# Kernel tuning notes

Measured on AMD Instinct MI355X. Metric: run time of the kernel, lower is better.

The kernel has to match this reference:

```python
import jax, jax.numpy as jnp
import numpy as np

N_NODES = 100000


def gcn_conv(x, W, b, src, dst, n_nodes):
    # PyG GCNConv: x' = D^{-1/2} (A + I) D^{-1/2} (x W) + b, deg counts self-loops
    h = x @ W  # [N, out]
    deg = jax.ops.segment_sum(jnp.ones_like(dst, dtype=h.dtype), dst, num_segments=n_nodes) + 1.0
    dinv = jax.lax.rsqrt(deg)  # [N]
    norm = dinv[src] * dinv[dst]  # per-edge norm [E]
    msg = h[src] * norm[:, None]  # gather + scale, [E, out]
    agg = jax.ops.segment_sum(msg, dst, num_segments=n_nodes)
    agg = agg + h * (dinv * dinv)[:, None]  # self-loop contribution
    return agg + b


def setup_inputs() -> dict:
    key = jax.random.key(0)
    ks = jax.random.split(key, 9)
    N, E, D = N_NODES, 3200000, 165
    x = jax.random.normal(ks[0], (N, D), dtype=jnp.float32)
    edge_index = jax.random.randint(ks[1], (2, E), 0, N, dtype=jnp.int64)
    def glorot(k, fan_in, fan_out):
        lim = np.sqrt(6.0 / (fan_in + fan_out))
        return jax.random.uniform(k, (fan_in, fan_out), jnp.float32, -lim, lim)
    return {
        "x": x,
        "edge_index": edge_index,
        "W1": glorot(ks[2], D, 32), "b1": jnp.zeros((32,), jnp.float32),
        "W2": glorot(ks[3], 32, 16), "b2": jnp.zeros((16,), jnp.float32),
        "W3": glorot(ks[4], 16, 2),  "b3": jnp.zeros((2,), jnp.float32),
    }


def reference(x, edge_index, W1, b1, W2, b2, W3, b3):
    src, dst = edge_index[0], edge_index[1]
    n = x.shape[0]
    h = jax.nn.relu(gcn_conv(x, W1, b1, src, dst, n))
    # dropout p=0.3 is a no-op in eval mode (training=False)
    h = jax.nn.relu(gcn_conv(h, W2, b2, src, dst, n))
    h = gcn_conv(h, W3, b3, src, dst, n)
    return jax.nn.log_softmax(h, axis=1)
```

## Files before the change

### kernel.cpp

```cpp
#include <hip/hip_runtime.h>
#include <math.h>


constexpr int NT = 256;
constexpr int NPB = 256;
constexpr int LOG_NPB = 8;
constexpr int MAXBUK = 512;
constexpr int BSTRIDE = 10240;
constexpr int NREP = 8;
constexpr int SUB = BSTRIDE / NREP;
constexpr int EPB_B = 4096;

typedef __attribute__((ext_vector_type(8))) short bf16x8;
typedef __attribute__((ext_vector_type(4))) float f32x4;

__device__ inline unsigned short f2bf(float f) {
    unsigned u = *(unsigned*)&f;
    u += 0x7fffu + ((u >> 16) & 1u);
    return (unsigned short)(u >> 16);
}
__device__ inline unsigned packbf(float a, float b) {
    return (unsigned)f2bf(a) | ((unsigned)f2bf(b) << 16);
}

__global__ __launch_bounds__(NT) void place_kernel(const int* __restrict__ src,
                                                   const int* __restrict__ dst,
                                                   int* __restrict__ cursor8,
                                                   unsigned* __restrict__ ebuf,
                                                   int E, int nbuk) {
    __shared__ int lh[MAXBUK];
    __shared__ int lbase[MAXBUK];
    for (int i = threadIdx.x; i < nbuk; i += NT) lh[i] = 0;
    __syncthreads();
    constexpr int EPT = EPB_B / NT;
    unsigned pk[EPT];
    unsigned bl[EPT];
    int base = blockIdx.x * EPB_B;
    int rep = blockIdx.x & (NREP - 1);
#pragma unroll
    for (int i = 0; i < EPT; i++) {
        int e = base + i * NT + threadIdx.x;
        if (e < E) {
            int s = src[e], d = dst[e];
            int b = d >> LOG_NPB;
            int lp = atomicAdd(&lh[b], 1);
            pk[i] = ((unsigned)(d & (NPB - 1)) << 24) | (unsigned)s;
            bl[i] = ((unsigned)b << 16) | (unsigned)lp;
        } else {
            bl[i] = 0xFFFFFFFFu;
        }
    }
    __syncthreads();
    for (int i = threadIdx.x; i < nbuk; i += NT) {
        int v = lh[i];
        if (v) lbase[i] = atomicAdd(&cursor8[rep * MAXBUK + i], v);
    }
    __syncthreads();
#pragma unroll
    for (int i = 0; i < EPT; i++) {
        if (bl[i] != 0xFFFFFFFFu) {
            int b = (int)(bl[i] >> 16);
            int pos = lbase[b] + (int)(bl[i] & 0xFFFFu);
            if (pos < SUB)
                ebuf[(size_t)b * BSTRIDE + rep * SUB + pos] = pk[i];
        }
    }
}

__global__ __launch_bounds__(NT) void sort_kernel(
    const unsigned* __restrict__ ebuf, const int* __restrict__ cursor8,
    int* __restrict__ esrc, int* __restrict__ rowptr, int* __restrict__ rowcnt,
    float* __restrict__ dinv, int N) {
    __shared__ int cnt[NPB];
    __shared__ int ofs[NPB];
    __shared__ int cur[NPB];
    int tid = threadIdx.x;
    int b = blockIdx.x;
    cnt[tid] = 0;
    __syncthreads();
#pragma unroll
    for (int r = 0; r < NREP; r++) {
        int e0 = b * BSTRIDE + r * SUB;
        int e1 = e0 + min(cursor8[r * MAXBUK + b], SUB);
        for (int i = e0 + tid; i < e1; i += NT)
            atomicAdd(&cnt[ebuf[i] >> 24], 1);
    }
    __syncthreads();
    ofs[tid] = cnt[tid];
    __syncthreads();
    for (int off = 1; off < NPB; off <<= 1) {
        int a = (tid >= off) ? ofs[tid - off] : 0;
        __syncthreads();
        ofs[tid] += a;
        __syncthreads();
    }
    {
        int excl = ofs[tid] - cnt[tid];
        cur[tid] = excl;
        int n = b * NPB + tid;
        if (n < N) {
            rowptr[n] = b * BSTRIDE + excl;
            rowcnt[n] = cnt[tid];
            dinv[n] = rsqrtf((float)cnt[tid] + 1.0f);
        }
    }
    __syncthreads();
#pragma unroll
    for (int r = 0; r < NREP; r++) {
        int e0 = b * BSTRIDE + r * SUB;
        int e1 = e0 + min(cursor8[r * MAXBUK + b], SUB);
        for (int i = e0 + tid; i < e1; i += NT) {
            unsigned p = ebuf[i];
            int l = (int)(p >> 24);
            int pos = atomicAdd(&cur[l], 1);
            esrc[b * BSTRIDE + pos] = (int)(p & 0xFFFFFFu);
        }
    }
}

__global__ __launch_bounds__(NT) void gemm1_mfma(
    const float* __restrict__ in, const float* __restrict__ W,
    const float* __restrict__ dinv, uint4* __restrict__ hs, int Ntot) {
    constexpr int DIN = 165, DOUT = 32;
    __shared__ float tile[4][16][36];
    int lane = threadIdx.x & 63;
    int wv = threadIdx.x >> 6;
    int t = blockIdx.x * 4 + wv;
    int ntiles = (Ntot + 15) >> 4;
    if (t >= ntiles) return;
    int n0 = t << 4;
    int mrow = lane & 15;
    int quad = lane >> 4;
    int arow = n0 + mrow;
    if (arow >= Ntot) arow = Ntot - 1;
    const float* xrow = in + (size_t)arow * DIN;
    f32x4 acc0 = {0.f, 0.f, 0.f, 0.f};
    f32x4 acc1 = {0.f, 0.f, 0.f, 0.f};
#pragma unroll
    for (int c = 0; c < 6; c++) {
        int kb = c * 32 + quad * 8;
        union { bf16x8 v; unsigned short u[8]; } A, B0, B1;
#pragma unroll
        for (int j = 0; j < 8; j++) {
            int k = kb + j;
            float xv = (k < DIN) ? xrow[k] : 0.f;
            float w0 = (k < DIN) ? W[k * DOUT + mrow] : 0.f;
            float w1 = (k < DIN) ? W[k * DOUT + 16 + mrow] : 0.f;
            A.u[j] = f2bf(xv);
            B0.u[j] = f2bf(w0);
            B1.u[j] = f2bf(w1);
        }
        acc0 = __builtin_amdgcn_mfma_f32_16x16x32_bf16(A.v, B0.v, acc0, 0, 0, 0);
        acc1 = __builtin_amdgcn_mfma_f32_16x16x32_bf16(A.v, B1.v, acc1, 0, 0, 0);
    }
#pragma unroll
    for (int r = 0; r < 4; r++) {
        tile[wv][quad * 4 + r][mrow] = acc0[r];
        tile[wv][quad * 4 + r][16 + mrow] = acc1[r];
    }
    int node = lane >> 2;
    int part = lane & 3;
    int n = n0 + node;
    if (n >= Ntot) return;
    float dv = dinv[n];
    float f[8];
#pragma unroll
    for (int i = 0; i < 8; i++) f[i] = tile[wv][node][part * 8 + i];
    unsigned u0 = packbf(dv * f[0], dv * f[1]);
    unsigned u1 = packbf(dv * f[2], dv * f[3]);
    unsigned u2 = packbf(dv * f[4], dv * f[5]);
    unsigned u3 = packbf(dv * f[6], dv * f[7]);
    int ch = part >> 1;
    int half = part & 1;
    hs[((size_t)ch * Ntot + n) * 2 + half] = make_uint4(u0, u1, u2, u3);
}

template <int DIN, int DOUT, int OUT>
__global__ __launch_bounds__(NT) void gemm_kernel(
    const float* __restrict__ in, const float* __restrict__ bprev,
    const float* __restrict__ W, const float* __restrict__ dinv,
    void* __restrict__ hs, int N) {
    int n = blockIdx.x * NT + threadIdx.x;
    if (n >= N) return;
    float dv = dinv[n];
    float acc[DOUT];
#pragma unroll
    for (int d = 0; d < DOUT; d++) acc[d] = 0.f;
    const float4* row4 = (const float4*)(in + (size_t)n * DIN);
#pragma unroll
    for (int q = 0; q < DIN / 4; q++) {
        float4 v = row4[q];
        float xv[4] = {v.x, v.y, v.z, v.w};
#pragma unroll
        for (int j = 0; j < 4; j++) {
            int k = q * 4 + j;
            float f = fmaxf(fmaf(dv, xv[j], bprev[k]), 0.f);
#pragma unroll
            for (int d = 0; d < DOUT; d++)
                acc[d] = fmaf(f, W[k * DOUT + d], acc[d]);
        }
    }
    if constexpr (OUT == 1) {
        unsigned u[8];
#pragma unroll
        for (int i = 0; i < 8; i++)
            u[i] = packbf(dv * acc[2 * i], dv * acc[2 * i + 1]);
        uint4* hp = (uint4*)hs + (size_t)n * 2;
        hp[0] = make_uint4(u[0], u[1], u[2], u[3]);
        hp[1] = make_uint4(u[4], u[5], u[6], u[7]);
    } else {
        float2 h = {dv * acc[0], dv * acc[1]};
        *(float2*)((float*)hs + (size_t)n * 2) = h;
    }
}

__global__ __launch_bounds__(NT) void gather1_kernel(
    const uint4* __restrict__ hsC, const int* __restrict__ esrc,
    const int* __restrict__ rowptr, const int* __restrict__ rowcnt,
    float4* __restrict__ aggBase, int strideF4, int baseOfs, int N) {
    int gid = blockIdx.x * NT + threadIdx.x;
    int n = gid >> 1;
    int c = gid & 1;
    if (n >= N) return;
    int j = rowptr[n];
    int end = j + rowcnt[n];
    float a[8];
    {
        uint4 v = hsC[(size_t)n * 2 + c];
        const unsigned* u = (const unsigned*)&v;
#pragma unroll
        for (int q = 0; q < 4; q++) {
            unsigned lo = u[q] << 16, hi = u[q] & 0xffff0000u;
            a[2 * q] = *(float*)&lo;
            a[2 * q + 1] = *(float*)&hi;
        }
    }
    for (; j + 4 <= end; j += 4) {
        uint4 v0 = hsC[(size_t)esrc[j] * 2 + c];
        uint4 v1 = hsC[(size_t)esrc[j + 1] * 2 + c];
        uint4 v2 = hsC[(size_t)esrc[j + 2] * 2 + c];
        uint4 v3 = hsC[(size_t)esrc[j + 3] * 2 + c];
        const uint4 vv[4] = {v0, v1, v2, v3};
#pragma unroll
        for (int m = 0; m < 4; m++) {
            const unsigned* u = (const unsigned*)&vv[m];
#pragma unroll
            for (int q = 0; q < 4; q++) {
                unsigned lo = u[q] << 16, hi = u[q] & 0xffff0000u;
                a[2 * q] += *(float*)&lo;
                a[2 * q + 1] += *(float*)&hi;
            }
        }
    }
    for (; j < end; j++) {
        uint4 v = hsC[(size_t)esrc[j] * 2 + c];
        const unsigned* u = (const unsigned*)&v;
#pragma unroll
        for (int q = 0; q < 4; q++) {
            unsigned lo = u[q] << 16, hi = u[q] & 0xffff0000u;
            a[2 * q] += *(float*)&lo;
            a[2 * q + 1] += *(float*)&hi;
        }
    }
    float4* ap = aggBase + (size_t)n * strideF4 + baseOfs + c * 2;
    ap[0] = make_float4(a[0], a[1], a[2], a[3]);
    ap[1] = make_float4(a[4], a[5], a[6], a[7]);
}

__global__ __launch_bounds__(NT) void final_kernel(
    const float* __restrict__ hs3, const int* __restrict__ esrc,
    const int* __restrict__ rowptr, const int* __restrict__ rowcnt,
    const float* __restrict__ dinv, const float* __restrict__ b,
    float* __restrict__ out, int N) {
    int n = blockIdx.x * NT + threadIdx.x;
    if (n >= N) return;
    int j = rowptr[n];
    int end = j + rowcnt[n];
    const float2* h2 = (const float2*)hs3;
    float2 acc = h2[n];
    for (; j + 4 <= end; j += 4) {
        float2 v0 = h2[esrc[j]], v1 = h2[esrc[j + 1]];
        float2 v2 = h2[esrc[j + 2]], v3 = h2[esrc[j + 3]];
        acc.x += v0.x + v1.x + v2.x + v3.x;
        acc.y += v0.y + v1.y + v2.y + v3.y;
    }
    for (; j < end; j++) {
        float2 v = h2[esrc[j]];
        acc.x += v.x; acc.y += v.y;
    }
    float dv = dinv[n];
    float z0 = fmaf(dv, acc.x, b[0]);
    float z1 = fmaf(dv, acc.y, b[1]);
    float m = fmaxf(z0, z1);
    float lse = m + logf(expf(z0 - m) + expf(z1 - m));
    out[(size_t)n * 2 + 0] = z0 - lse;
    out[(size_t)n * 2 + 1] = z1 - lse;
}

extern "C" void kernel_launch(void* const* d_in, const int* in_sizes, int n_in,
                              void* d_out, int out_size, void* d_ws, size_t ws_size,
                              hipStream_t stream) {
    const float* x  = (const float*)d_in[0];
    const int*   ei = (const int*)d_in[1];
    const float* W1 = (const float*)d_in[2];
    const float* b1 = (const float*)d_in[3];
    const float* W2 = (const float*)d_in[4];
    const float* b2 = (const float*)d_in[5];
    const float* W3 = (const float*)d_in[6];
    const float* b3 = (const float*)d_in[7];
    float* out = (float*)d_out;

    const int N = in_sizes[0] / 165;
    const int E = in_sizes[1] / 2;
    const int* src = ei;
    const int* dst = ei + E;
    const int nbuk = (N + NPB - 1) >> LOG_NPB;
    const int NB = (N + NT - 1) / NT;

    char* p = (char*)d_ws;
    int* cursor8   = (int*)p;      p += (size_t)NREP * MAXBUK * 4;
    unsigned* ebuf = (unsigned*)p; p += (size_t)nbuk * BSTRIDE * 4;
    int* esrc      = (int*)p;      p += (size_t)nbuk * BSTRIDE * 4;
    int* rowptr    = (int*)p;      p += (size_t)N * 4;
    int* rowcnt    = (int*)p;      p += (size_t)N * 4;
    float* dinv    = (float*)p;    p += (size_t)N * 4;
    uint4* hs1b    = (uint4*)p;    p += (size_t)N * 16 * 4;
    float* agg1    = (float*)p;    p += (size_t)N * 32 * 4;
    uint4* hs2b    = (uint4*)p;    p += (size_t)N * 8 * 4;
    float* hs3     = (float*)p;    p += (size_t)N * 2 * 4;
    float* agg2    = (float*)hs1b;

    hipMemsetAsync(cursor8, 0, (size_t)NREP * MAXBUK * sizeof(int), stream);
    place_kernel<<<(E + EPB_B - 1) / EPB_B, NT, 0, stream>>>(src, dst, cursor8, ebuf, E, nbuk);
    sort_kernel<<<nbuk, NT, 0, stream>>>(ebuf, cursor8, esrc, rowptr, rowcnt, dinv, N);

    const int GB = ((size_t)N * 2 + NT - 1) / NT;

    gemm1_mfma<<<((N + 15) / 16 + 3) / 4, NT, 0, stream>>>(x, W1, dinv, hs1b, N);
    for (int ch = 0; ch < 2; ch++) {
        gather1_kernel<<<GB, NT, 0, stream>>>(
            hs1b + (size_t)ch * N * 2, esrc, rowptr, rowcnt,
            (float4*)agg1, 8, ch * 4, N);
    }

    gemm_kernel<32, 16, 1><<<NB, NT, 0, stream>>>(agg1, b1, W2, dinv, hs2b, N);
    gather1_kernel<<<GB, NT, 0, stream>>>(
        hs2b, esrc, rowptr, rowcnt, (float4*)agg2, 4, 0, N);

    gemm_kernel<16, 2, 0><<<NB, NT, 0, stream>>>(agg2, b2, W3, dinv, hs3, N);
    final_kernel<<<NB, NT, 0, stream>>>(hs3, esrc, rowptr, rowcnt, dinv, b3, out, N);
}
```

Before: 327.5 us.

## Replace CSR sort with bucket-level LDS atomic aggregation

Drops the per-node counting sort that built the esrc/rowptr arrays. Each 256-node bucket block now walks its unsorted edge bucket directly and accumulates neighbour features into shared memory with float atomics. The sort kernel becomes a degree-only kernel, and the layer-1 hs layout changes to row-contiguous so one thread gathers the full 32 features. This removes the sort pass and its esrc traffic, but adds LDS atomic contention. It also makes float summation order nondeterministic and leaves only about 196 blocks of 512 threads to cover the GPU.

```diff
diff --git a/kernel.cpp b/kernel.cpp
--- a/kernel.cpp
+++ b/kernel.cpp
@@ -10,6 +10,7 @@
 constexpr int NREP = 8;
 constexpr int SUB = BSTRIDE / NREP;
 constexpr int EPB_B = 4096;
+constexpr int AT = 512;
 
 typedef __attribute__((ext_vector_type(8))) short bf16x8;
 typedef __attribute__((ext_vector_type(4))) float f32x4;
@@ -21,6 +22,9 @@
 }
 __device__ inline unsigned packbf(float a, float b) {
     return (unsigned)f2bf(a) | ((unsigned)f2bf(b) << 16);
+}
+__device__ inline void lds_fadd(float* p, float v) {
+    __hip_atomic_fetch_add(p, v, __ATOMIC_RELAXED, __HIP_MEMORY_SCOPE_WORKGROUP);
 }
 
 __global__ __launch_bounds__(NT) void place_kernel(const int* __restrict__ src,
@@ -67,13 +71,10 @@
     }
 }
 
-__global__ __launch_bounds__(NT) void sort_kernel(
+__global__ __launch_bounds__(NT) void degree_kernel(
     const unsigned* __restrict__ ebuf, const int* __restrict__ cursor8,
-    int* __restrict__ esrc, int* __restrict__ rowptr, int* __restrict__ rowcnt,
     float* __restrict__ dinv, int N) {
     __shared__ int cnt[NPB];
-    __shared__ int ofs[NPB];
-    __shared__ int cur[NPB];
     int tid = threadIdx.x;
     int b = blockIdx.x;
     cnt[tid] = 0;
@@ -86,36 +87,8 @@
             atomicAdd(&cnt[ebuf[i] >> 24], 1);
     }
     __syncthreads();
-    ofs[tid] = cnt[tid];
-    __syncthreads();
-    for (int off = 1; off < NPB; off <<= 1) {
-        int a = (tid >= off) ? ofs[tid - off] : 0;
-        __syncthreads();
-        ofs[tid] += a;
-        __syncthreads();
-    }
-    {
-        int excl = ofs[tid] - cnt[tid];
-        cur[tid] = excl;
-        int n = b * NPB + tid;
-        if (n < N) {
-            rowptr[n] = b * BSTRIDE + excl;
-            rowcnt[n] = cnt[tid];
-            dinv[n] = rsqrtf((float)cnt[tid] + 1.0f);
-        }
-    }
-    __syncthreads();
-#pragma unroll
-    for (int r = 0; r < NREP; r++) {
-        int e0 = b * BSTRIDE + r * SUB;
-        int e1 = e0 + min(cursor8[r * MAXBUK + b], SUB);
-        for (int i = e0 + tid; i < e1; i += NT) {
-            unsigned p = ebuf[i];
-            int l = (int)(p >> 24);
-            int pos = atomicAdd(&cur[l], 1);
-            esrc[b * BSTRIDE + pos] = (int)(p & 0xFFFFFFu);
-        }
-    }
+    int n = b * NPB + tid;
+    if (n < N) dinv[n] = rsqrtf((float)cnt[tid] + 1.0f);
 }
 
 __global__ __launch_bounds__(NT) void gemm1_mfma(
@@ -170,9 +143,7 @@
     unsigned u1 = packbf(dv * f[2], dv * f[3]);
     unsigned u2 = packbf(dv * f[4], dv * f[5]);
     unsigned u3 = packbf(dv * f[6], dv * f[7]);
-    int ch = part >> 1;
-    int half = part & 1;
-    hs[((size_t)ch * Ntot + n) * 2 + half] = make_uint4(u0, u1, u2, u3);
+    hs[(size_t)n * 4 + part] = make_uint4(u0, u1, u2, u3);
 }
 
 template <int DIN, int DOUT, int OUT>
@@ -214,87 +185,92 @@
     }
 }
 
-__global__ __launch_bounds__(NT) void gather1_kernel(
-    const uint4* __restrict__ hsC, const int* __restrict__ esrc,
-    const int* __restrict__ rowptr, const int* __restrict__ rowcnt,
-    float4* __restrict__ aggBase, int strideF4, int baseOfs, int N) {
-    int gid = blockIdx.x * NT + threadIdx.x;
-    int n = gid >> 1;
-    int c = gid & 1;
-    if (n >= N) return;
-    int j = rowptr[n];
-    int end = j + rowcnt[n];
-    float a[8];
-    {
-        uint4 v = hsC[(size_t)n * 2 + c];
+template <int NF>
+__global__ __launch_bounds__(AT) void agg_kernel(
+    const uint4* __restrict__ hsb, const unsigned* __restrict__ ebuf,
+    const int* __restrict__ cursor8, float* __restrict__ aggOut, int N) {
+    constexpr int NQ = NF / 8;
+    __shared__ float acc[NF][NPB];
+    int tid = threadIdx.x;
+    int b = blockIdx.x;
+    for (int i = tid; i < NF * NPB; i += AT) (&acc[0][0])[i] = 0.f;
+    __syncthreads();
+#pragma unroll
+    for (int r = 0; r < NREP; r++) {
+        int e0 = b * BSTRIDE + r * SUB;
+        int e1 = e0 + min(cursor8[r * MAXBUK + b], SUB);
+        for (int i = e0 + tid; i < e1; i += AT) {
+            unsigned pk = ebuf[i];
+            int l = (int)(pk >> 24);
+            const uint4* hp = hsb + (size_t)(pk & 0xFFFFFFu) * NQ;
+#pragma unroll
+            for (int q = 0; q < NQ; q++) {
+                uint4 v = hp[q];
+                const unsigned* u = (const unsigned*)&v;
+#pragma unroll
+                for (int w = 0; w < 4; w++) {
+                    unsigned lo = u[w] << 16, hi = u[w] & 0xffff0000u;
+                    lds_fadd(&acc[q * 8 + 2 * w][l], *(float*)&lo);
+                    lds_fadd(&acc[q * 8 + 2 * w + 1][l], *(float*)&hi);
+                }
+            }
+        }
+    }
+    __syncthreads();
+    for (int idx = tid; idx < NPB * NQ; idx += AT) {
+        int l = idx / NQ, q = idx % NQ;
+        int n = b * NPB + l;
+        if (n >= N) continue;
+        uint4 v = hsb[(size_t)n * NQ + q];
         const unsigned* u = (const unsigned*)&v;
-#pragma unroll
-        for (int q = 0; q < 4; q++) {
-            unsigned lo = u[q] << 16, hi = u[q] & 0xffff0000u;
-            a[2 * q] = *(float*)&lo;
-            a[2 * q + 1] = *(float*)&hi;
-        }
-    }
-    for (; j + 4 <= end; j += 4) {
-        uint4 v0 = hsC[(size_t)esrc[j] * 2 + c];
-        uint4 v1 = hsC[(size_t)esrc[j + 1] * 2 + c];
-        uint4 v2 = hsC[(size_t)esrc[j + 2] * 2 + c];
-        uint4 v3 = hsC[(size_t)esrc[j + 3] * 2 + c];
-        const uint4 vv[4] = {v0, v1, v2, v3};
-#pragma unroll
-        for (int m = 0; m < 4; m++) {
-            const unsigned* u = (const unsigned*)&vv[m];
-#pragma unroll
-            for (int q = 0; q < 4; q++) {
-                unsigned lo = u[q] << 16, hi = u[q] & 0xffff0000u;
-                a[2 * q] += *(float*)&lo;
-                a[2 * q + 1] += *(float*)&hi;
-            }
-        }
-    }
-    for (; j < end; j++) {
-        uint4 v = hsC[(size_t)esrc[j] * 2 + c];
-        const unsigned* u = (const unsigned*)&v;
-#pragma unroll
-        for (int q = 0; q < 4; q++) {
-            unsigned lo = u[q] << 16, hi = u[q] & 0xffff0000u;
-            a[2 * q] += *(float*)&lo;
-            a[2 * q + 1] += *(float*)&hi;
-        }
-    }
-    float4* ap = aggBase + (size_t)n * strideF4 + baseOfs + c * 2;
-    ap[0] = make_float4(a[0], a[1], a[2], a[3]);
-    ap[1] = make_float4(a[4], a[5], a[6], a[7]);
-}
-
-__global__ __launch_bounds__(NT) void final_kernel(
-    const float* __restrict__ hs3, const int* __restrict__ esrc,
-    const int* __restrict__ rowptr, const int* __restrict__ rowcnt,
-    const float* __restrict__ dinv, const float* __restrict__ b,
-    float* __restrict__ out, int N) {
-    int n = blockIdx.x * NT + threadIdx.x;
-    if (n >= N) return;
-    int j = rowptr[n];
-    int end = j + rowcnt[n];
-    const float2* h2 = (const float2*)hs3;
-    float2 acc = h2[n];
-    for (; j + 4 <= end; j += 4) {
-        float2 v0 = h2[esrc[j]], v1 = h2[esrc[j + 1]];
-        float2 v2 = h2[esrc[j + 2]], v3 = h2[esrc[j + 3]];
-        acc.x += v0.x + v1.x + v2.x + v3.x;
-        acc.y += v0.y + v1.y + v2.y + v3.y;
-    }
-    for (; j < end; j++) {
-        float2 v = h2[esrc[j]];
-        acc.x += v.x; acc.y += v.y;
-    }
-    float dv = dinv[n];
-    float z0 = fmaf(dv, acc.x, b[0]);
-    float z1 = fmaf(dv, acc.y, b[1]);
-    float m = fmaxf(z0, z1);
-    float lse = m + logf(expf(z0 - m) + expf(z1 - m));
-    out[(size_t)n * 2 + 0] = z0 - lse;
-    out[(size_t)n * 2 + 1] = z1 - lse;
+        float o[8];
+#pragma unroll
+        for (int w = 0; w < 4; w++) {
+            unsigned lo = u[w] << 16, hi = u[w] & 0xffff0000u;
+            o[2 * w]     = acc[q * 8 + 2 * w][l]     + *(float*)&lo;
+            o[2 * w + 1] = acc[q * 8 + 2 * w + 1][l] + *(float*)&hi;
+        }
+        float4* ap = (float4*)(aggOut + (size_t)n * NF + q * 8);
+        ap[0] = make_float4(o[0], o[1], o[2], o[3]);
+        ap[1] = make_float4(o[4], o[5], o[6], o[7]);
+    }
+}
+
+__global__ __launch_bounds__(AT) void agg3_kernel(
+    const float* __restrict__ hs3, const unsigned* __restrict__ ebuf,
+    const int* __restrict__ cursor8, const float* __restrict__ dinv,
+    const float* __restrict__ bias, float* __restrict__ out, int N) {
+    __shared__ float acc0[NPB];
+    __shared__ float acc1[NPB];
+    int tid = threadIdx.x;
+    int b = blockIdx.x;
+    for (int i = tid; i < NPB; i += AT) { acc0[i] = 0.f; acc1[i] = 0.f; }
+    __syncthreads();
+#pragma unroll
+    for (int r = 0; r < NREP; r++) {
+        int e0 = b * BSTRIDE + r * SUB;
+        int e1 = e0 + min(cursor8[r * MAXBUK + b], SUB);
+        for (int i = e0 + tid; i < e1; i += AT) {
+            unsigned pk = ebuf[i];
+            int l = (int)(pk >> 24);
+            float2 v = ((const float2*)hs3)[pk & 0xFFFFFFu];
+            lds_fadd(&acc0[l], v.x);
+            lds_fadd(&acc1[l], v.y);
+        }
+    }
+    __syncthreads();
+    for (int l = tid; l < NPB; l += AT) {
+        int n = b * NPB + l;
+        if (n >= N) continue;
+        float2 self = ((const float2*)hs3)[n];
+        float dv = dinv[n];
+        float z0 = fmaf(dv, acc0[l] + self.x, bias[0]);
+        float z1 = fmaf(dv, acc1[l] + self.y, bias[1]);
+        float m = fmaxf(z0, z1);
+        float lse = m + logf(expf(z0 - m) + expf(z1 - m));
+        out[(size_t)n * 2 + 0] = z0 - lse;
+        out[(size_t)n * 2 + 1] = z1 - lse;
+    }
 }
 
 extern "C" void kernel_launch(void* const* d_in, const int* in_sizes, int n_in,
@@ -320,33 +296,23 @@
     char* p = (char*)d_ws;
     int* cursor8   = (int*)p;      p += (size_t)NREP * MAXBUK * 4;
     unsigned* ebuf = (unsigned*)p; p += (size_t)nbuk * BSTRIDE * 4;
-    int* esrc      = (int*)p;      p += (size_t)nbuk * BSTRIDE * 4;
-    int* rowptr    = (int*)p;      p += (size_t)N * 4;
-    int* rowcnt    = (int*)p;      p += (size_t)N * 4;
     float* dinv    = (float*)p;    p += (size_t)N * 4;
-    uint4* hs1b    = (uint4*)p;    p += (size_t)N * 16 * 4;
+    uint4* hs1b    = (uint4*)p;    p += (size_t)N * 4 * 16;
     float* agg1    = (float*)p;    p += (size_t)N * 32 * 4;
-    uint4* hs2b    = (uint4*)p;    p += (size_t)N * 8 * 4;
+    uint4* hs2b    = (uint4*)p;    p += (size_t)N * 2 * 16;
     float* hs3     = (float*)p;    p += (size_t)N * 2 * 4;
     float* agg2    = (float*)hs1b;
 
     hipMemsetAsync(cursor8, 0, (size_t)NREP * MAXBUK * sizeof(int), stream);
     place_kernel<<<(E + EPB_B - 1) / EPB_B, NT, 0, stream>>>(src, dst, cursor8, ebuf, E, nbuk);
-    sort_kernel<<<nbuk, NT, 0, stream>>>(ebuf, cursor8, esrc, rowptr, rowcnt, dinv, N);
-
-    const int GB = ((size_t)N * 2 + NT - 1) / NT;
+    degree_kernel<<<nbuk, NT, 0, stream>>>(ebuf, cursor8, dinv, N);
 
     gemm1_mfma<<<((N + 15) / 16 + 3) / 4, NT, 0, stream>>>(x, W1, dinv, hs1b, N);
-    for (int ch = 0; ch < 2; ch++) {
-        gather1_kernel<<<GB, NT, 0, stream>>>(
-            hs1b + (size_t)ch * N * 2, esrc, rowptr, rowcnt,
-            (float4*)agg1, 8, ch * 4, N);
-    }
+    agg_kernel<32><<<nbuk, AT, 0, stream>>>(hs1b, ebuf, cursor8, agg1, N);
 
     gemm_kernel<32, 16, 1><<<NB, NT, 0, stream>>>(agg1, b1, W2, dinv, hs2b, N);
-    gather1_kernel<<<GB, NT, 0, stream>>>(
-        hs2b, esrc, rowptr, rowcnt, (float4*)agg2, 4, 0, N);
+    agg_kernel<16><<<nbuk, AT, 0, stream>>>(hs2b, ebuf, cursor8, agg2, N);
 
     gemm_kernel<16, 2, 0><<<NB, NT, 0, stream>>>(agg2, b2, W3, dinv, hs3, N);
-    final_kernel<<<NB, NT, 0, stream>>>(hs3, esrc, rowptr, rowcnt, dinv, b3, out, N);
-}
+    agg3_kernel<<<nbuk, AT, 0, stream>>>(hs3, ebuf, cursor8, dinv, b3, out, N);
+}
```

After: 1.243 ms. 280% more time.

## Fuse neighbor aggregation with next-layer dense transform and interleave layer-1 features

Applied to the files above, without the earlier changes.

Each neighbor-gather kernel now applies bias, ReLU and the next layer's small weight matrix in-register, with two threads per node reducing partial products via a lane shuffle. This removes the fp32 agg1/agg2 round-trips through global memory and two separate gemm launches. The layer-1 bf16 features change from two channel-split planes to a node-interleaved layout, so one pass gathers all 32 features as two contiguous 16-byte loads instead of running the gather twice. The cost is more registers per thread, plus W2 and b2 staged in shared memory in every block.

```diff
diff --git a/kernel.cpp b/kernel.cpp
--- a/kernel.cpp
+++ b/kernel.cpp
@@ -21,6 +21,15 @@
 }
 __device__ inline unsigned packbf(float a, float b) {
     return (unsigned)f2bf(a) | ((unsigned)f2bf(b) << 16);
+}
+__device__ inline void acc8(float* a, uint4 v) {
+    const unsigned* u = (const unsigned*)&v;
+#pragma unroll
+    for (int w = 0; w < 4; w++) {
+        unsigned lo = u[w] << 16, hi = u[w] & 0xffff0000u;
+        a[2 * w]     += *(float*)&lo;
+        a[2 * w + 1] += *(float*)&hi;
+    }
 }
 
 __global__ __launch_bounds__(NT) void place_kernel(const int* __restrict__ src,
@@ -170,54 +179,87 @@
     unsigned u1 = packbf(dv * f[2], dv * f[3]);
     unsigned u2 = packbf(dv * f[4], dv * f[5]);
     unsigned u3 = packbf(dv * f[6], dv * f[7]);
-    int ch = part >> 1;
-    int half = part & 1;
-    hs[((size_t)ch * Ntot + n) * 2 + half] = make_uint4(u0, u1, u2, u3);
-}
-
-template <int DIN, int DOUT, int OUT>
-__global__ __launch_bounds__(NT) void gemm_kernel(
-    const float* __restrict__ in, const float* __restrict__ bprev,
-    const float* __restrict__ W, const float* __restrict__ dinv,
-    void* __restrict__ hs, int N) {
-    int n = blockIdx.x * NT + threadIdx.x;
+    hs[(size_t)n * 4 + part] = make_uint4(u0, u1, u2, u3);
+}
+
+__global__ __launch_bounds__(NT) void g1g2_kernel(
+    const uint4* __restrict__ hsb, const int* __restrict__ esrc,
+    const int* __restrict__ rowptr, const int* __restrict__ rowcnt,
+    const float* __restrict__ dinv, const float* __restrict__ b1,
+    const float* __restrict__ W2 , uint4* __restrict__ hs2b,
+    int N) {
+    __shared__ float sW[32 * 16];
+    __shared__ float sb[32];
+    for (int i = threadIdx.x; i < 32 * 16; i += NT) sW[i] = W2[i];
+    if (threadIdx.x < 32) sb[threadIdx.x] = b1[threadIdx.x];
+    __syncthreads();
+    int gid = blockIdx.x * NT + threadIdx.x;
+    int n = gid >> 1;
+    int c = gid & 1;
     if (n >= N) return;
+    int j = rowptr[n];
+    int end = j + rowcnt[n];
+    float a[16];
+    {
+        const uint4* hp = hsb + (size_t)n * 4 + c * 2;
+        uint4 v0 = hp[0], v1 = hp[1];
+        const unsigned* u0 = (const unsigned*)&v0;
+        const unsigned* u1 = (const unsigned*)&v1;
+#pragma unroll
+        for (int w = 0; w < 4; w++) {
+            unsigned lo = u0[w] << 16, hi = u0[w] & 0xffff0000u;
+            a[2 * w] = *(float*)&lo; a[2 * w + 1] = *(float*)&hi;
+            unsigned lo1 = u1[w] << 16, hi1 = u1[w] & 0xffff0000u;
+            a[8 + 2 * w] = *(float*)&lo1; a[8 + 2 * w + 1] = *(float*)&hi1;
+        }
+    }
+    for (; j + 4 <= end; j += 4) {
+        int s0 = esrc[j], s1 = esrc[j + 1], s2 = esrc[j + 2], s3 = esrc[j + 3];
+        uint4 v00 = hsb[(size_t)s0 * 4 + c * 2], v01 = hsb[(size_t)s0 * 4 + c * 2 + 1];
+        uint4 v10 = hsb[(size_t)s1 * 4 + c * 2], v11 = hsb[(size_t)s1 * 4 + c * 2 + 1];
+        uint4 v20 = hsb[(size_t)s2 * 4 + c * 2], v21 = hsb[(size_t)s2 * 4 + c * 2 + 1];
+        uint4 v30 = hsb[(size_t)s3 * 4 + c * 2], v31 = hsb[(size_t)s3 * 4 + c * 2 + 1];
+        acc8(a, v00); acc8(a + 8, v01);
+        acc8(a, v10); acc8(a + 8, v11);
+        acc8(a, v20); acc8(a + 8, v21);
+        acc8(a, v30); acc8(a + 8, v31);
+    }
+    for (; j < end; j++) {
+        int s = esrc[j];
+        acc8(a, hsb[(size_t)s * 4 + c * 2]);
+        acc8(a + 8, hsb[(size_t)s * 4 + c * 2 + 1]);
+    }
     float dv = dinv[n];
-    float acc[DOUT];
-#pragma unroll
-    for (int d = 0; d < DOUT; d++) acc[d] = 0.f;
-    const float4* row4 = (const float4*)(in + (size_t)n * DIN);
-#pragma unroll
-    for (int q = 0; q < DIN / 4; q++) {
-        float4 v = row4[q];
-        float xv[4] = {v.x, v.y, v.z, v.w};
-#pragma unroll
-        for (int j = 0; j < 4; j++) {
-            int k = q * 4 + j;
-            float f = fmaxf(fmaf(dv, xv[j], bprev[k]), 0.f);
-#pragma unroll
-            for (int d = 0; d < DOUT; d++)
-                acc[d] = fmaf(f, W[k * DOUT + d], acc[d]);
-        }
-    }
-    if constexpr (OUT == 1) {
-        unsigned u[8];
-#pragma unroll
-        for (int i = 0; i < 8; i++)
-            u[i] = packbf(dv * acc[2 * i], dv * acc[2 * i + 1]);
-        uint4* hp = (uint4*)hs + (size_t)n * 2;
-        hp[0] = make_uint4(u[0], u[1], u[2], u[3]);
-        hp[1] = make_uint4(u[4], u[5], u[6], u[7]);
-    } else {
-        float2 h = {dv * acc[0], dv * acc[1]};
-        *(float2*)((float*)hs + (size_t)n * 2) = h;
-    }
-}
-
-__global__ __launch_bounds__(NT) void gather1_kernel(
-    const uint4* __restrict__ hsC, const int* __restrict__ esrc,
+    float z[16];
+#pragma unroll
+    for (int d = 0; d < 16; d++) z[d] = 0.f;
+#pragma unroll
+    for (int k = 0; k < 16; k++) {
+        float f = fmaxf(fmaf(dv, a[k], sb[c * 16 + k]), 0.f);
+#pragma unroll
+        for (int d = 0; d < 16; d++)
+            z[d] = fmaf(f, sW[(c * 16 + k) * 16 + d], z[d]);
+    }
+#pragma unroll
+    for (int d = 0; d < 16; d++) z[d] += __shfl_xor(z[d], 1);
+    unsigned u0 = packbf(dv * z[c * 8 + 0], dv * z[c * 8 + 1]);
+    unsigned u1 = packbf(dv * z[c * 8 + 2], dv * z[c * 8 + 3]);
+    unsigned u2 = packbf(dv * z[c * 8 + 4], dv * z[c * 8 + 5]);
+    unsigned u3 = packbf(dv * z[c * 8 + 6], dv * z[c * 8 + 7]);
+    hs2b[(size_t)n * 2 + c] = make_uint4(u0, u1, u2, u3);
+}
+
+__global__ __launch_bounds__(NT) void g2g3_kernel(
+    const uint4* __restrict__ hs2b, const int* __restrict__ esrc,
     const int* __restrict__ rowptr, const int* __restrict__ rowcnt,
-    float4* __restrict__ aggBase, int strideF4, int baseOfs, int N) {
+    const float* __restrict__ dinv, const float* __restrict__ b2,
+    const float* __restrict__ W3 , float* __restrict__ hs3,
+    int N) {
+    __shared__ float sW[32];
+    __shared__ float sb[16];
+    if (threadIdx.x < 32) sW[threadIdx.x] = W3[threadIdx.x];
+    if (threadIdx.x < 16) sb[threadIdx.x] = b2[threadIdx.x];
+    __syncthreads();
     int gid = blockIdx.x * NT + threadIdx.x;
     int n = gid >> 1;
     int c = gid & 1;
@@ -226,45 +268,36 @@
     int end = j + rowcnt[n];
     float a[8];
     {
-        uint4 v = hsC[(size_t)n * 2 + c];
+        uint4 v = hs2b[(size_t)n * 2 + c];
         const unsigned* u = (const unsigned*)&v;
 #pragma unroll
-        for (int q = 0; q < 4; q++) {
-            unsigned lo = u[q] << 16, hi = u[q] & 0xffff0000u;
-            a[2 * q] = *(float*)&lo;
-            a[2 * q + 1] = *(float*)&hi;
+        for (int w = 0; w < 4; w++) {
+            unsigned lo = u[w] << 16, hi = u[w] & 0xffff0000u;
+            a[2 * w] = *(float*)&lo; a[2 * w + 1] = *(float*)&hi;
         }
     }
     for (; j + 4 <= end; j += 4) {
-        uint4 v0 = hsC[(size_t)esrc[j] * 2 + c];
-        uint4 v1 = hsC[(size_t)esrc[j + 1] * 2 + c];
-        uint4 v2 = hsC[(size_t)esrc[j + 2] * 2 + c];
-        uint4 v3 = hsC[(size_t)esrc[j + 3] * 2 + c];
-        const uint4 vv[4] = {v0, v1, v2, v3};
-#pragma unroll
-        for (int m = 0; m < 4; m++) {
-            const unsigned* u = (const unsigned*)&vv[m];
-#pragma unroll
-            for (int q = 0; q < 4; q++) {
-                unsigned lo = u[q] << 16, hi = u[q] & 0xffff0000u;
-                a[2 * q] += *(float*)&lo;
-                a[2 * q + 1] += *(float*)&hi;
-            }
-        }
-    }
-    for (; j < end; j++) {
-        uint4 v = hsC[(size_t)esrc[j] * 2 + c];
-        const unsigned* u = (const unsigned*)&v;
-#pragma unroll
-        for (int q = 0; q < 4; q++) {
-            unsigned lo = u[q] << 16, hi = u[q] & 0xffff0000u;
-            a[2 * q] += *(float*)&lo;
-            a[2 * q + 1] += *(float*)&hi;
-        }
-    }
-    float4* ap = aggBase + (size_t)n * strideF4 + baseOfs + c * 2;
-    ap[0] = make_float4(a[0], a[1], a[2], a[3]);
-    ap[1] = make_float4(a[4], a[5], a[6], a[7]);
+        uint4 v0 = hs2b[(size_t)esrc[j] * 2 + c];
+        uint4 v1 = hs2b[(size_t)esrc[j + 1] * 2 + c];
+        uint4 v2 = hs2b[(size_t)esrc[j + 2] * 2 + c];
+        uint4 v3 = hs2b[(size_t)esrc[j + 3] * 2 + c];
+        acc8(a, v0); acc8(a, v1); acc8(a, v2); acc8(a, v3);
+    }
+    for (; j < end; j++) acc8(a, hs2b[(size_t)esrc[j] * 2 + c]);
+    float dv = dinv[n];
+    float z0 = 0.f, z1 = 0.f;
+#pragma unroll
+    for (int k = 0; k < 8; k++) {
+        float f = fmaxf(fmaf(dv, a[k], sb[c * 8 + k]), 0.f);
+        z0 = fmaf(f, sW[(c * 8 + k) * 2 + 0], z0);
+        z1 = fmaf(f, sW[(c * 8 + k) * 2 + 1], z1);
+    }
+    z0 += __shfl_xor(z0, 1);
+    z1 += __shfl_xor(z1, 1);
+    if (c == 0) {
+        hs3[(size_t)n * 2 + 0] = dv * z0;
+        hs3[(size_t)n * 2 + 1] = dv * z1;
+    }
 }
 
 __global__ __launch_bounds__(NT) void final_kernel(
@@ -316,6 +349,7 @@
     const int* dst = ei + E;
     const int nbuk = (N + NPB - 1) >> LOG_NPB;
     const int NB = (N + NT - 1) / NT;
+    const int GB = ((size_t)N * 2 + NT - 1) / NT;
 
     char* p = (char*)d_ws;
     int* cursor8   = (int*)p;      p += (size_t)NREP * MAXBUK * 4;
@@ -324,29 +358,19 @@
     int* rowptr    = (int*)p;      p += (size_t)N * 4;
     int* rowcnt    = (int*)p;      p += (size_t)N * 4;
     float* dinv    = (float*)p;    p += (size_t)N * 4;
-    uint4* hs1b    = (uint4*)p;    p += (size_t)N * 16 * 4;
-    float* agg1    = (float*)p;    p += (size_t)N * 32 * 4;
-    uint4* hs2b    = (uint4*)p;    p += (size_t)N * 8 * 4;
+    uint4* hs1b    = (uint4*)p;    p += (size_t)N * 4 * 16;
+    uint4* hs2b    = (uint4*)p;    p += (size_t)N * 2 * 16;
     float* hs3     = (float*)p;    p += (size_t)N * 2 * 4;
-    float* agg2    = (float*)hs1b;
-
-    hipMemsetAsync(cursor8, 0, (size_t)NREP * MAXBUK * sizeof(int), stream);
+
+    (void)hipMemsetAsync(cursor8, 0, (size_t)NREP * MAXBUK * sizeof(int), stream);
     place_kernel<<<(E + EPB_B - 1) / EPB_B, NT, 0, stream>>>(src, dst, cursor8, ebuf, E, nbuk);
     sort_kernel<<<nbuk, NT, 0, stream>>>(ebuf, cursor8, esrc, rowptr, rowcnt, dinv, N);
 
-    const int GB = ((size_t)N * 2 + NT - 1) / NT;
-
     gemm1_mfma<<<((N + 15) / 16 + 3) / 4, NT, 0, stream>>>(x, W1, dinv, hs1b, N);
-    for (int ch = 0; ch < 2; ch++) {
-        gather1_kernel<<<GB, NT, 0, stream>>>(
-            hs1b + (size_t)ch * N * 2, esrc, rowptr, rowcnt,
-            (float4*)agg1, 8, ch * 4, N);
-    }
-
-    gemm_kernel<32, 16, 1><<<NB, NT, 0, stream>>>(agg1, b1, W2, dinv, hs2b, N);
-    gather1_kernel<<<GB, NT, 0, stream>>>(
-        hs2b, esrc, rowptr, rowcnt, (float4*)agg2, 4, 0, N);
-
-    gemm_kernel<16, 2, 0><<<NB, NT, 0, stream>>>(agg2, b2, W3, dinv, hs3, N);
+
+    g1g2_kernel<<<GB, NT, 0, stream>>>(hs1b, esrc, rowptr, rowcnt, dinv, b1, W2, hs2b, N);
+
+    g2g3_kernel<<<GB, NT, 0, stream>>>(hs2b, esrc, rowptr, rowcnt, dinv, b2, W3, hs3, N);
+
     final_kernel<<<NB, NT, 0, stream>>>(hs3, esrc, rowptr, rowcnt, dinv, b3, out, N);
 }
```

Result: faster. 293.9 us (-10.2%).
